# Performance work log

Measured on AMD Instinct MI355X. Metric: run time of the kernel, lower is better.

The kernel has to match this reference:

```python
import jax, jax.numpy as jnp
import numpy as np


def setup_inputs() -> dict:
    key = jax.random.key(0)
    k1, k2, k3, k4 = jax.random.split(key, 4)
    Q = jax.random.normal(k1, (32, 32, 128), dtype=jnp.float32)
    D = jax.random.normal(k2, (512, 180, 128), dtype=jnp.float32)
    q_mask = jax.random.randint(k3, (32, 32), 0, 2, dtype=jnp.int32)
    d_mask = jax.random.randint(k4, (512, 180), 0, 2, dtype=jnp.int32)
    return {"Q": Q, "D": D, "q_mask": q_mask, "d_mask": d_mask}


def reference(Q, D, q_mask, d_mask):
    # ColBERT MaxSim late-interaction scoring (ColBERT_List_qa.score)
    # Q: [q, m, h], D: [d, n, h]; masks zero out padding token embeddings.
    Qm = Q * q_mask.astype(Q.dtype)[..., None]              # [q, m, h]
    Dm = D * d_mask.astype(D.dtype)[..., None]              # [d, n, h]
    sim = jnp.einsum("qmh,dnh->qdmn", Qm, Dm)               # [q, d, m, n]
    scores = sim.max(axis=-1).sum(axis=-1)                  # max over doc tokens n, sum over query tokens m -> [q, d]
    return scores
```

## Files before the change

kernel.cpp:

```cpp
#include <hip/hip_runtime.h>
#include <hip/hip_bf16.h>

typedef __attribute__((ext_vector_type(8))) short short8;
typedef __attribute__((ext_vector_type(4))) float f32x4;

#define NQ 32
#define NM 32
#define NH 128
#define ND 512
#define NN 180
#define NTMAX 12

#define QFRAG_BYTES (NQ * 2 * 4 * 64 * 16)

static __device__ __forceinline__ unsigned short f2bf(float x) {
  __hip_bfloat16 h = __float2bfloat16(x);
  return __builtin_bit_cast(unsigned short, h);
}

static __device__ __forceinline__ uint4 pack8m(const float* v, float m) {
  unsigned int a = (unsigned)f2bf(v[0] * m) | ((unsigned)f2bf(v[1] * m) << 16);
  unsigned int b = (unsigned)f2bf(v[2] * m) | ((unsigned)f2bf(v[3] * m) << 16);
  unsigned int c = (unsigned)f2bf(v[4] * m) | ((unsigned)f2bf(v[5] * m) << 16);
  unsigned int e = (unsigned)f2bf(v[6] * m) | ((unsigned)f2bf(v[7] * m) << 16);
  return make_uint4(a, b, c, e);
}

static __device__ __forceinline__ uint4 pack8(float4 a, float4 b) {
  unsigned int x = (unsigned)f2bf(a.x) | ((unsigned)f2bf(a.y) << 16);
  unsigned int y = (unsigned)f2bf(a.z) | ((unsigned)f2bf(a.w) << 16);
  unsigned int z = (unsigned)f2bf(b.x) | ((unsigned)f2bf(b.y) << 16);
  unsigned int u = (unsigned)f2bf(b.z) | ((unsigned)f2bf(b.w) << 16);
  return make_uint4(x, y, z, u);
}


__global__ __launch_bounds__(256) void prep_q_frag(
    const float* __restrict__ Q, const int* __restrict__ qmask,
    unsigned short* __restrict__ Qb) {
  int idx = blockIdx.x * 256 + threadIdx.x;
  int lane = idx & 63;
  int ks = (idx >> 6) & 3;
  int mt = (idx >> 8) & 1;
  int q  = idx >> 9;
  int row = mt * 16 + (lane & 15);
  int k0  = ks * 32 + (lane >> 4) * 8;
  const float* src = Q + (q * NM + row) * NH + k0;
  float v[8];
  *reinterpret_cast<float4*>(&v[0]) = *reinterpret_cast<const float4*>(src);
  *reinterpret_cast<float4*>(&v[4]) = *reinterpret_cast<const float4*>(src + 4);
  float m = (float)qmask[q * NM + row];
  reinterpret_cast<uint4*>(Qb)[idx] = pack8m(v, m);
}

__global__ __launch_bounds__(512, 4) void fused_maxsim(
    const float* __restrict__ D, const int* __restrict__ dmask,
    const unsigned short* __restrict__ Qb, float* __restrict__ out) {
  __shared__ unsigned char Dlds[NTMAX * 4096];
  __shared__ unsigned short mapinv[192];
  __shared__ int wtot[4];
  const int d = blockIdx.x;
  const int tid = threadIdx.x;
  const int lane = tid & 63;
  const int w = tid >> 6;
  const float NEG = -__builtin_inff();

  int flag = 0, pre = 0;
  if (tid < NN) flag = dmask[d * NN + tid];
  if (tid < 192) {
    unsigned long long bal = __ballot(flag != 0);
    pre = __popcll(bal & ((1ull << lane) - 1ull));
    if (lane == 63) wtot[w] = pre + (flag ? 1 : 0);
  }
  __syncthreads();
  const int cnt = wtot[0] + wtot[1] + wtot[2];
  if (tid < 192 && flag) {
    int base = (w >= 1 ? wtot[0] : 0) + (w >= 2 ? wtot[1] : 0);
    mapinv[pre + base] = (unsigned short)tid;
  }
  __syncthreads();

  const int ntc = (cnt + 15) >> 4;
  for (int s = tid; s < ntc * 256; s += 512) {
    int nt = s >> 8, ks = (s >> 6) & 3, ln = s & 63;
    int bl = ln & 15, bg2 = ln >> 4;
    int dr = nt * 16 + bl;
    uint4 o = make_uint4(0u, 0u, 0u, 0u);
    if (dr < cnt) {
      int sr = mapinv[dr];
      const float4* p = reinterpret_cast<const float4*>(D) +
                        (size_t)(d * NN + sr) * 32 + ks * 8 + bg2 * 2;
      o = pack8(p[0], p[1]);
    }
    *reinterpret_cast<uint4*>(&Dlds[(size_t)s * 16]) = o;
  }
  __syncthreads();

  const int bg = lane >> 4;

  #pragma unroll 1
  for (int p = 0; p < 2; ++p) {
    const int q0 = w * 4 + p * 2;

    short8 Qf[2][2][4];
    #pragma unroll
    for (int qi = 0; qi < 2; ++qi)
      #pragma unroll
      for (int mt = 0; mt < 2; ++mt)
        #pragma unroll
        for (int ks = 0; ks < 4; ++ks)
          Qf[qi][mt][ks] = *reinterpret_cast<const short8*>(
              reinterpret_cast<const char*>(Qb) +
              ((((q0 + qi) * 2 + mt) * 4 + ks) << 10) + (lane << 4));

    float run[2][2];
    #pragma unroll
    for (int qi = 0; qi < 2; ++qi)
      #pragma unroll
      for (int mt = 0; mt < 2; ++mt) run[qi][mt] = NEG;

    #pragma unroll 2
    for (int nt = 0; nt < ntc; ++nt) {
      short8 Da[4];
      #pragma unroll
      for (int ks = 0; ks < 4; ++ks)
        Da[ks] = *reinterpret_cast<const short8*>(
            &Dlds[((nt * 4 + ks) << 10) + (lane << 4)]);

      f32x4 acc[2][2];
      #pragma unroll
      for (int qi = 0; qi < 2; ++qi)
        #pragma unroll
        for (int mt = 0; mt < 2; ++mt) acc[qi][mt] = (f32x4){0.f, 0.f, 0.f, 0.f};

      #pragma unroll
      for (int ks = 0; ks < 4; ++ks)
        #pragma unroll
        for (int qi = 0; qi < 2; ++qi)
          #pragma unroll
          for (int mt = 0; mt < 2; ++mt)
            acc[qi][mt] = __builtin_amdgcn_mfma_f32_16x16x32_bf16(
                Da[ks], Qf[qi][mt][ks], acc[qi][mt], 0, 0, 0);

      if (nt * 16 + 16 > cnt) {
        const int rlim = cnt - nt * 16 - bg * 4;
        #pragma unroll
        for (int qi = 0; qi < 2; ++qi)
          #pragma unroll
          for (int mt = 0; mt < 2; ++mt) {
            float vmax = NEG;
            #pragma unroll
            for (int j = 0; j < 4; ++j) {
              float v = (j < rlim) ? acc[qi][mt][j] : NEG;
              vmax = fmaxf(vmax, v);
            }
            run[qi][mt] = fmaxf(run[qi][mt], vmax);
          }
      } else {
        #pragma unroll
        for (int qi = 0; qi < 2; ++qi)
          #pragma unroll
          for (int mt = 0; mt < 2; ++mt) {
            float vmax = fmaxf(fmaxf(acc[qi][mt][0], acc[qi][mt][1]),
                               fmaxf(acc[qi][mt][2], acc[qi][mt][3]));
            run[qi][mt] = fmaxf(run[qi][mt], vmax);
          }
      }
    }

    if (cnt < NN) {
      #pragma unroll
      for (int qi = 0; qi < 2; ++qi)
        #pragma unroll
        for (int mt = 0; mt < 2; ++mt) run[qi][mt] = fmaxf(run[qi][mt], 0.f);
    }

    #pragma unroll
    for (int qi = 0; qi < 2; ++qi) {
      float a = run[qi][0];
      float bb = run[qi][1];
      a = fmaxf(a, __shfl_xor(a, 16));
      a = fmaxf(a, __shfl_xor(a, 32));
      bb = fmaxf(bb, __shfl_xor(bb, 16));
      bb = fmaxf(bb, __shfl_xor(bb, 32));
      float s = a + bb;
      s += __shfl_xor(s, 1);
      s += __shfl_xor(s, 2);
      s += __shfl_xor(s, 4);
      s += __shfl_xor(s, 8);
      if (lane == 0) out[(q0 + qi) * ND + d] = s;
    }
  }
}

extern "C" void kernel_launch(void* const* d_in, const int* in_sizes, int n_in,
                              void* d_out, int out_size, void* d_ws, size_t ws_size,
                              hipStream_t stream) {
  const float* Q = (const float*)d_in[0];
  const float* D = (const float*)d_in[1];
  const int* qmask = (const int*)d_in[2];
  const int* dmask = (const int*)d_in[3];
  float* out = (float*)d_out;
  unsigned short* Qb = (unsigned short*)d_ws;

  prep_q_frag<<<16384 / 256, 256, 0, stream>>>(Q, qmask, Qb);
  fused_maxsim<<<ND, 512, 0, stream>>>(D, dmask, Qb, out);
}
```

Baseline: 25.90 us.

## Precompute doc compaction maps in prep kernel and split queries across two blocks

The dmask compaction (ballot/prefix) moves into the prep kernel, which writes per-document index maps and counts to workspace. The main kernel now launches two 256-thread blocks per document, each covering half the queries, with a d/qh interleaved block mapping. Each block loads and converts all 12 tiles unconditionally, without checking against cnt, so the D tile load is duplicated across both halves. The intent is more blocks for better occupancy and no in-kernel ballot or extra syncs, at the cost of converting D to bf16 twice and doing more global reads.

Result: slower. 29.45 us (+13.7%).

```diff
diff --git a/kernel.cpp b/kernel.cpp
--- a/kernel.cpp
+++ b/kernel.cpp
@@ -12,6 +12,8 @@
 #define NTMAX 12
 
 #define QFRAG_BYTES (NQ * 2 * 4 * 64 * 16)
+#define MAPINV_OFF  QFRAG_BYTES
+#define CNT_OFF     (MAPINV_OFF + ND * 192 * 2)
 
 static __device__ __forceinline__ unsigned short f2bf(float x) {
   __hip_bfloat16 h = __float2bfloat16(x);
@@ -34,73 +36,88 @@
   return make_uint4(x, y, z, u);
 }
 
-
-__global__ __launch_bounds__(256) void prep_q_frag(
+__global__ __launch_bounds__(256) void prep_kernel(
     const float* __restrict__ Q, const int* __restrict__ qmask,
-    unsigned short* __restrict__ Qb) {
-  int idx = blockIdx.x * 256 + threadIdx.x;
-  int lane = idx & 63;
-  int ks = (idx >> 6) & 3;
-  int mt = (idx >> 8) & 1;
-  int q  = idx >> 9;
-  int row = mt * 16 + (lane & 15);
-  int k0  = ks * 32 + (lane >> 4) * 8;
-  const float* src = Q + (q * NM + row) * NH + k0;
-  float v[8];
-  *reinterpret_cast<float4*>(&v[0]) = *reinterpret_cast<const float4*>(src);
-  *reinterpret_cast<float4*>(&v[4]) = *reinterpret_cast<const float4*>(src + 4);
-  float m = (float)qmask[q * NM + row];
-  reinterpret_cast<uint4*>(Qb)[idx] = pack8m(v, m);
-}
-
-__global__ __launch_bounds__(512, 4) void fused_maxsim(
-    const float* __restrict__ D, const int* __restrict__ dmask,
-    const unsigned short* __restrict__ Qb, float* __restrict__ out) {
-  __shared__ unsigned char Dlds[NTMAX * 4096];
-  __shared__ unsigned short mapinv[192];
-  __shared__ int wtot[4];
-  const int d = blockIdx.x;
+    const int* __restrict__ dmask, unsigned short* __restrict__ Qb,
+    unsigned short* __restrict__ mapinv_g, int* __restrict__ cnt_arr) {
+  const int tid = threadIdx.x;
+
+  if (blockIdx.x < 64) {
+    int idx = blockIdx.x * 256 + tid;
+    int lane = idx & 63;
+    int ks = (idx >> 6) & 3;
+    int mt = (idx >> 8) & 1;
+    int q  = idx >> 9;
+    int row = mt * 16 + (lane & 15);
+    int k0  = ks * 32 + (lane >> 4) * 8;
+    const float* src = Q + (q * NM + row) * NH + k0;
+    float v[8];
+    *reinterpret_cast<float4*>(&v[0]) = *reinterpret_cast<const float4*>(src);
+    *reinterpret_cast<float4*>(&v[4]) = *reinterpret_cast<const float4*>(src + 4);
+    float m = (float)qmask[q * NM + row];
+    reinterpret_cast<uint4*>(Qb)[idx] = pack8m(v, m);
+  } else {
+    __shared__ int wtot[3];
+    const int d = blockIdx.x - 64;
+    const int lane = tid & 63;
+    const int w = tid >> 6;
+
+    int flag = 0, pre = 0;
+    if (tid < NN) flag = dmask[d * NN + tid];
+    if (tid < 192) {
+      unsigned long long bal = __ballot(flag != 0);
+      pre = __popcll(bal & ((1ull << lane) - 1ull));
+      if (lane == 63) wtot[w] = pre + (flag ? 1 : 0);
+    }
+    __syncthreads();
+    const int cnt = wtot[0] + wtot[1] + wtot[2];
+    if (tid < 192 && tid >= cnt) mapinv_g[d * 192 + tid] = 0;
+    if (tid < 192 && flag) {
+      int base = (w >= 1 ? wtot[0] : 0) + (w >= 2 ? wtot[1] : 0);
+      mapinv_g[d * 192 + pre + base] = (unsigned short)tid;
+    }
+    if (tid == 0) cnt_arr[d] = cnt;
+  }
+}
+
+__global__ __launch_bounds__(256, 4) void fused_maxsim(
+    const float* __restrict__ D, const unsigned short* __restrict__ mapinv_g,
+    const int* __restrict__ cnt_arr, const unsigned short* __restrict__ Qb,
+    float* __restrict__ out) {
+  __shared__ __attribute__((aligned(16))) unsigned char Dlds[NTMAX * 4096];
+  const int bid = blockIdx.x;
+  const int d  = ((bid >> 4) << 3) | (bid & 7);
+  const int qh = (bid >> 3) & 1;
   const int tid = threadIdx.x;
   const int lane = tid & 63;
   const int w = tid >> 6;
+  const int bg = lane >> 4;
   const float NEG = -__builtin_inff();
 
-  int flag = 0, pre = 0;
-  if (tid < NN) flag = dmask[d * NN + tid];
-  if (tid < 192) {
-    unsigned long long bal = __ballot(flag != 0);
-    pre = __popcll(bal & ((1ull << lane) - 1ull));
-    if (lane == 63) wtot[w] = pre + (flag ? 1 : 0);
+  const int cnt = cnt_arr[d];
+  const int ntc = (cnt + 15) >> 4;
+
+  {
+    const unsigned short* mig = mapinv_g + d * 192;
+    const int sbl = tid & 15;
+    const int sks = tid >> 6;
+    const int sbg = (tid >> 4) & 3;
+    unsigned short srow[NTMAX];
+    #pragma unroll
+    for (int u = 0; u < NTMAX; ++u) srow[u] = mig[u * 16 + sbl];
+    #pragma unroll
+    for (int u = 0; u < NTMAX; ++u) {
+      const float4* p = reinterpret_cast<const float4*>(D) +
+                        (size_t)(d * NN + srow[u]) * 32 + sks * 8 + sbg * 2;
+      uint4 o = pack8(p[0], p[1]);
+      *reinterpret_cast<uint4*>(&Dlds[(size_t)(u * 256 + tid) * 16]) = o;
+    }
   }
   __syncthreads();
-  const int cnt = wtot[0] + wtot[1] + wtot[2];
-  if (tid < 192 && flag) {
-    int base = (w >= 1 ? wtot[0] : 0) + (w >= 2 ? wtot[1] : 0);
-    mapinv[pre + base] = (unsigned short)tid;
-  }
-  __syncthreads();
-
-  const int ntc = (cnt + 15) >> 4;
-  for (int s = tid; s < ntc * 256; s += 512) {
-    int nt = s >> 8, ks = (s >> 6) & 3, ln = s & 63;
-    int bl = ln & 15, bg2 = ln >> 4;
-    int dr = nt * 16 + bl;
-    uint4 o = make_uint4(0u, 0u, 0u, 0u);
-    if (dr < cnt) {
-      int sr = mapinv[dr];
-      const float4* p = reinterpret_cast<const float4*>(D) +
-                        (size_t)(d * NN + sr) * 32 + ks * 8 + bg2 * 2;
-      o = pack8(p[0], p[1]);
-    }
-    *reinterpret_cast<uint4*>(&Dlds[(size_t)s * 16]) = o;
-  }
-  __syncthreads();
-
-  const int bg = lane >> 4;
 
   #pragma unroll 1
   for (int p = 0; p < 2; ++p) {
-    const int q0 = w * 4 + p * 2;
+    const int q0 = qh * 16 + w * 4 + p * 2;
 
     short8 Qf[2][2][4];
     #pragma unroll
@@ -201,8 +218,11 @@
   const int* qmask = (const int*)d_in[2];
   const int* dmask = (const int*)d_in[3];
   float* out = (float*)d_out;
+
   unsigned short* Qb = (unsigned short*)d_ws;
-
-  prep_q_frag<<<16384 / 256, 256, 0, stream>>>(Q, qmask, Qb);
-  fused_maxsim<<<ND, 512, 0, stream>>>(D, dmask, Qb, out);
-}
+  unsigned short* mapinv_g = (unsigned short*)((char*)d_ws + MAPINV_OFF);
+  int* cnt_arr = (int*)((char*)d_ws + CNT_OFF);
+
+  prep_kernel<<<64 + ND, 256, 0, stream>>>(Q, qmask, dmask, Qb, mapinv_g, cnt_arr);
+  fused_maxsim<<<ND * 2, 256, 0, stream>>>(D, mapinv_g, cnt_arr, Qb, out);
+}
```
